# Optimization experiments

Measured on AMD Instinct MI355X. Metric: run time of the kernel, lower is better.

The kernel has to match this reference:

```python
import jax, jax.numpy as jnp
import numpy as np
import math

B, S, D, H = 1, 4096, 1024, 16
HD = D // H  # head_dim = 64


def setup_inputs() -> dict:
    key = jax.random.key(0)
    ks = jax.random.split(key, 6)
    x = jax.random.normal(ks[0], (B, S, D), dtype=jnp.float32)
    # Llama-style rotary frequencies: theta = 10000^{-2i/head_dim}
    inv_freq = 1.0 / (10000.0 ** (jnp.arange(0, HD, 2, dtype=jnp.float32) / HD))  # (HD/2,)
    t = jnp.arange(S, dtype=jnp.float32)
    freqs = jnp.outer(t, inv_freq)  # (S, HD/2)
    cos = jnp.cos(freqs)
    sin = jnp.sin(freqs)
    # additive causal mask (S, S): 0 on/below diagonal, -inf above
    mask = jnp.where(jnp.tril(jnp.ones((S, S), dtype=bool)), 0.0, -jnp.inf).astype(jnp.float32)
    scale = 1.0 / math.sqrt(D)
    wq = jax.random.normal(ks[1], (D, D), dtype=jnp.float32) * scale
    wk = jax.random.normal(ks[2], (D, D), dtype=jnp.float32) * scale
    wv = jax.random.normal(ks[3], (D, D), dtype=jnp.float32) * scale
    wo = jax.random.normal(ks[4], (D, D), dtype=jnp.float32) * scale
    return {"x": x, "cos": cos, "sin": sin, "mask": mask,
            "wq": wq, "wk": wk, "wv": wv, "wo": wo, "start_pos": 0}


def _rope(t, cos, sin):
    # t: (b, s, h, hd); cos/sin: (s, hd/2). Interleaved-pair complex rotation.
    b, s, h, hd = t.shape
    tr = t.reshape(b, s, h, hd // 2, 2)
    te, to = tr[..., 0], tr[..., 1]
    c = cos[None, :, None, :]
    sn = sin[None, :, None, :]
    oe = te * c - to * sn
    oo = te * sn + to * c
    return jnp.stack([oe, oo], axis=-1).reshape(b, s, h, hd)


def reference(x, cos, sin, mask, wq, wk, wv, wo, start_pos):
    b, s, d = x.shape
    h, hd = H, HD
    # Linear layers: y = x @ W.T (torch nn.Linear convention, W is (out,in))
    xq = (x @ wq.T).reshape(b, s, h, hd)
    xk = (x @ wk.T).reshape(b, s, h, hd)
    xv = (x @ wv.T).reshape(b, s, h, hd)
    xq = _rope(xq, cos, sin)
    xk = _rope(xk, cos, sin)
    # (b, h, s, hd)
    xq = xq.transpose(0, 2, 1, 3)
    xk = xk.transpose(0, 2, 1, 3)
    xv = xv.transpose(0, 2, 1, 3)
    scores = jnp.einsum('bhqd,bhkd->bhqk', xq, xk) / math.sqrt(hd)
    scores = scores + mask[None, None, :, :]
    attn = jax.nn.softmax(scores.astype(jnp.float32), axis=-1).astype(xq.dtype)
    out = jnp.einsum('bhqk,bhkd->bhqd', attn, xv)
    out = out.transpose(0, 2, 1, 3).reshape(b, s, d)
    return out @ wo.T
```

## Files before the change

kernel.cpp:

```cpp
#include <hip/hip_runtime.h>
#include <hip/hip_bf16.h>
#include <math.h>

typedef __bf16 bf16;
typedef __bf16 bf16x4 __attribute__((ext_vector_type(4)));
typedef __bf16 bf16x8 __attribute__((ext_vector_type(8)));
typedef float floatx4 __attribute__((ext_vector_type(4)));
typedef short short4v __attribute__((ext_vector_type(4)));

#define S_LEN 4096
#define DM 1024
#define NH 16
#define HD 64

#define GM 4096
#define GN 1024
#define GK 1024
#define FST 68

#define GLDS16(gp, lp) __builtin_amdgcn_global_load_lds( \
    (const __attribute__((address_space(1))) void*)(gp), \
    (__attribute__((address_space(3))) void*)(lp), 16, 0, 0)

__global__ void cvt_bf16(const float* __restrict__ x,  const float* __restrict__ wq,
                         const float* __restrict__ wk, const float* __restrict__ wv,
                         const float* __restrict__ wo, bf16* __restrict__ dst)
{
    size_t i4 = ((size_t)blockIdx.x * 256 + threadIdx.x) * 4;
    const float* src; size_t off;
    const size_t M1 = (size_t)1 << 20;
    if      (i4 < 4 * M1) { src = x;  off = i4;          }
    else if (i4 < 5 * M1) { src = wq; off = i4 - 4 * M1; }
    else if (i4 < 6 * M1) { src = wk; off = i4 - 5 * M1; }
    else if (i4 < 7 * M1) { src = wv; off = i4 - 6 * M1; }
    else                  { src = wo; off = i4 - 7 * M1; }
    float4 v = *(const float4*)(src + off);
    bf16x4 o = { (bf16)v.x, (bf16)v.y, (bf16)v.z, (bf16)v.w };
    *(bf16x4*)(&dst[i4]) = o;
}

template <typename CT>
__launch_bounds__(256)
__global__ void gemm_bt3(const bf16* __restrict__ A,
                         const bf16* __restrict__ B0, const bf16* __restrict__ B1,
                         const bf16* __restrict__ B2,
                         CT* __restrict__ C0, CT* __restrict__ C1, CT* __restrict__ C2)
{
    const int bz = blockIdx.z;
    const bf16* __restrict__ B = (bz == 0) ? B0 : (bz == 1 ? B1 : B2);
    CT* __restrict__ C         = (bz == 0) ? C0 : (bz == 1 ? C1 : C2);

    const int tid  = threadIdx.x;
    const int wave = tid >> 6;
    const int lane = tid & 63;
    const int wm   = (wave >> 1) * 64;
    const int wn   = (wave & 1) * 64;
    const int lrow = lane >> 4;
    const int lcol = lane & 15;

    const int m0 = blockIdx.y * 128;
    const int n0 = blockIdx.x * 128;

    __shared__ __align__(16) bf16 As[128 * 64];
    __shared__ __align__(16) bf16 Bs[128 * 64];

    floatx4 acc[4][4];
    #pragma unroll
    for (int i = 0; i < 4; i++)
        #pragma unroll
        for (int j = 0; j < 4; j++) acc[i][j] = (floatx4){0.f, 0.f, 0.f, 0.f};

    const bf16* ga0 = A + (size_t)(m0 + wave * 32 + (lane >> 3)) * GK + (lane & 7) * 8;
    const bf16* gb0 = B + (size_t)(n0 + wave * 32 + (lane >> 3)) * GK + (lane & 7) * 8;
    bf16* la = &As[(wave * 32) * 64];
    bf16* lb = &Bs[(wave * 32) * 64];

    for (int kt = 0; kt < GK; kt += 64) {
        #pragma unroll
        for (int i = 0; i < 4; i++) {
            GLDS16(ga0 + kt + (size_t)i * 8 * GK, la + i * 8 * 64);
            GLDS16(gb0 + kt + (size_t)i * 8 * GK, lb + i * 8 * 64);
        }
        __syncthreads();
        #pragma unroll
        for (int ks = 0; ks < 2; ks++) {
            bf16x8 af[4], bfr[4];
            #pragma unroll
            for (int t = 0; t < 4; t++) {
                af[t]  = *(const bf16x8*)(&As[(wm + t * 16 + lcol) * 64 + ks * 32 + lrow * 8]);
                bfr[t] = *(const bf16x8*)(&Bs[(wn + t * 16 + lcol) * 64 + ks * 32 + lrow * 8]);
            }
            #pragma unroll
            for (int mt = 0; mt < 4; mt++)
                #pragma unroll
                for (int nt = 0; nt < 4; nt++)
                    acc[mt][nt] = __builtin_amdgcn_mfma_f32_16x16x32_bf16(af[mt], bfr[nt], acc[mt][nt], 0, 0, 0);
        }
        __syncthreads();
    }

    #pragma unroll
    for (int mt = 0; mt < 4; mt++)
        #pragma unroll
        for (int nt = 0; nt < 4; nt++)
            #pragma unroll
            for (int r = 0; r < 4; r++) {
                int row = m0 + wm + mt * 16 + lrow * 4 + r;
                int col = n0 + wn + nt * 16 + lcol;
                C[(size_t)row * GN + col] = (CT)(acc[mt][nt][r]);
            }
}

__global__ void rope_kernel(bf16* __restrict__ Q, bf16* __restrict__ Kp,
                            const float* __restrict__ cosp, const float* __restrict__ sinp)
{
    int idx = blockIdx.x * 256 + threadIdx.x;
    int s = idx >> 9;
    int r = idx & 511;
    int h = r >> 5;
    int i = r & 31;
    float c  = cosp[s * 32 + i];
    float sn = sinp[s * 32 + i];
    int base = s * DM + h * 64 + 2 * i;
    float qe = (float)Q[base], qo = (float)Q[base + 1];
    Q[base]      = (bf16)(qe * c - qo * sn);
    Q[base + 1]  = (bf16)(qe * sn + qo * c);
    float ke = (float)Kp[base], ko = (float)Kp[base + 1];
    Kp[base]     = (bf16)(ke * c - ko * sn);
    Kp[base + 1] = (bf16)(ke * sn + ko * c);
}

__global__ void vtrans_kernel(const bf16* __restrict__ V, bf16* __restrict__ VT)
{
    __shared__ bf16 T[64 * 70];
    const int tid = threadIdx.x;
    const int s0  = blockIdx.x * 64;
    const int h   = blockIdx.y;
    #pragma unroll
    for (int i = 0; i < 2; i++) {
        int idx = i * 256 + tid;
        int r   = idx >> 3;
        int c   = (idx & 7) * 8;
        *(uint4*)(&T[r * 70 + c]) = *(const uint4*)(&V[(size_t)(s0 + r) * DM + h * 64 + c]);
    }
    __syncthreads();
    #pragma unroll
    for (int i = 0; i < 2; i++) {
        int idx = i * 256 + tid;
        int d   = idx >> 3;
        int c0  = (idx & 7) * 8;
        bf16x8 o;
        #pragma unroll
        for (int j = 0; j < 8; j++) o[j] = T[(c0 + j) * 70 + d];
        *(bf16x8*)(&VT[(size_t)(h * 64 + d) * S_LEN + s0 + c0]) = o;
    }
}

__launch_bounds__(256)
__global__ void flash_attn(const bf16* __restrict__ Q, const bf16* __restrict__ K,
                           const bf16* __restrict__ VT, bf16* __restrict__ O)
{
    const int bx   = blockIdx.x;
    const int h    = blockIdx.y;
    const int tid  = threadIdx.x;
    const int wave = tid >> 6;
    const int lane = tid & 63;
    const int lrow = lane >> 4;
    const int lcol = lane & 15;

    __shared__ __align__(16) bf16 Ks[2][64 * FST];
    __shared__ __align__(16) bf16 Vs[2][64 * FST];

    const float sc2 = 0.125f * 1.44269504088896340736f;

    const int  srow = tid >> 3;
    const int  sch  = (tid & 7) * 8;
    const bf16* kp  = K  + (size_t)srow * DM + h * HD + sch;
    const bf16* vp  = VT + (size_t)(h * HD + srow) * S_LEN + sch;
    const int  wof  = srow * FST + sch;

    for (int pass = 0; pass < 2; pass++) {
        const int qt = pass ? (63 - bx) : bx;
        const int q0 = qt * 64 + wave * 16;

        const bf16* qptr = Q + (size_t)(q0 + lcol) * DM + h * HD;
        bf16x8 qf[2];
        qf[0] = *(const bf16x8*)(qptr + 0 * 32 + lrow * 8);
        qf[1] = *(const bf16x8*)(qptr + 1 * 32 + lrow * 8);

        float l_lane = 0.f;
        floatx4 oacc[4];
        #pragma unroll
        for (int nt = 0; nt < 4; nt++) oacc[nt] = (floatx4){0.f, 0.f, 0.f, 0.f};

        uint4 kr0 = *(const uint4*)(kp);
        uint4 kr1 = *(const uint4*)(kp + (size_t)32 * DM);
        uint4 vr0 = *(const uint4*)(vp);
        uint4 vr1 = *(const uint4*)(vp + (size_t)32 * S_LEN);
        *(uint4*)(&Ks[0][wof])            = kr0;
        *(uint4*)(&Ks[0][wof + 32 * FST]) = kr1;
        *(uint4*)(&Vs[0][wof])            = vr0;
        *(uint4*)(&Vs[0][wof + 32 * FST]) = vr1;
        __syncthreads();

        const int ntiles = qt + 1;
        for (int t = 0; t < ntiles; t++) {
            const int cur = t & 1;
            const bool more = (t + 1 < ntiles);

            if (more) {
                size_t ko = (size_t)(t + 1) * 64 * DM;
                size_t vo = (size_t)(t + 1) * 64;
                kr0 = *(const uint4*)(kp + ko);
                kr1 = *(const uint4*)(kp + ko + (size_t)32 * DM);
                vr0 = *(const uint4*)(vp + vo);
                vr1 = *(const uint4*)(vp + vo + (size_t)32 * S_LEN);
            }

            floatx4 st[4];
            #pragma unroll
            for (int nt = 0; nt < 4; nt++) {
                floatx4 z = (floatx4){0.f, 0.f, 0.f, 0.f};
                #pragma unroll
                for (int ks = 0; ks < 2; ks++) {
                    bf16x8 kf = *(const bf16x8*)(&Ks[cur][(nt * 16 + lcol) * FST + ks * 32 + lrow * 8]);
                    z = __builtin_amdgcn_mfma_f32_16x16x32_bf16(kf, qf[ks], z, 0, 0, 0);
                }
                st[nt] = z;
            }

            if (t == qt) {
                #pragma unroll
                for (int nt = 0; nt < 4; nt++)
                    #pragma unroll
                    for (int r = 0; r < 4; r++) {
                        int kg = t * 64 + nt * 16 + lrow * 4 + r;
                        int qg = q0 + lcol;
                        float p = exp2f(st[nt][r] * sc2);
                        if (kg > qg) p = 0.f;
                        st[nt][r] = p;
                        l_lane += p;
                    }
            } else {
                #pragma unroll
                for (int nt = 0; nt < 4; nt++)
                    #pragma unroll
                    for (int r = 0; r < 4; r++) {
                        float p = exp2f(st[nt][r] * sc2);
                        st[nt][r] = p;
                        l_lane += p;
                    }
            }

            short4v pb[4];
            #pragma unroll
            for (int kt = 0; kt < 4; kt++) {
                bf16x4 pv = { (bf16)st[kt][0], (bf16)st[kt][1],
                              (bf16)st[kt][2], (bf16)st[kt][3] };
                pb[kt] = __builtin_bit_cast(short4v, pv);
            }

            #pragma unroll
            for (int nt = 0; nt < 4; nt++)
                #pragma unroll
                for (int kt = 0; kt < 4; kt++) {
                    bf16x4 va = *(const bf16x4*)(&Vs[cur][(nt * 16 + lcol) * FST + kt * 16 + lrow * 4]);
                    oacc[nt] = __builtin_amdgcn_mfma_f32_16x16x16bf16_1k(
                        __builtin_bit_cast(short4v, va), pb[kt], oacc[nt], 0, 0, 0);
                }

            if (more) {
                int nxt = cur ^ 1;
                *(uint4*)(&Ks[nxt][wof])            = kr0;
                *(uint4*)(&Ks[nxt][wof + 32 * FST]) = kr1;
                *(uint4*)(&Vs[nxt][wof])            = vr0;
                *(uint4*)(&Vs[nxt][wof + 32 * FST]) = vr1;
            }
            __syncthreads();
        }

        float l = l_lane + __shfl_xor(l_lane, 16, 64);
        l += __shfl_xor(l, 32, 64);
        float rl = 1.f / l;

        #pragma unroll
        for (int nt = 0; nt < 4; nt++) {
            bf16x4 ov = { (bf16)(oacc[nt][0] * rl), (bf16)(oacc[nt][1] * rl),
                          (bf16)(oacc[nt][2] * rl), (bf16)(oacc[nt][3] * rl) };
            *(bf16x4*)(&O[(size_t)(q0 + lcol) * DM + h * HD + nt * 16 + lrow * 4]) = ov;
        }
    }
}

extern "C" void kernel_launch(void* const* d_in, const int* in_sizes, int n_in,
                              void* d_out, int out_size, void* d_ws, size_t ws_size,
                              hipStream_t stream) {
    const float* x    = (const float*)d_in[0];
    const float* cosp = (const float*)d_in[1];
    const float* sinp = (const float*)d_in[2];
    const float* wq   = (const float*)d_in[4];
    const float* wk   = (const float*)d_in[5];
    const float* wv   = (const float*)d_in[6];
    const float* wo   = (const float*)d_in[7];
    float* out = (float*)d_out;

    const size_t SD = (size_t)S_LEN * DM;
    const size_t DD = (size_t)DM * DM;
    bf16* xb  = (bf16*)d_ws;
    bf16* wqb = xb + SD;
    bf16* wkb = wqb + DD;
    bf16* wvb = wkb + DD;
    bf16* wob = wvb + DD;
    bf16* Qw  = wob + DD;
    bf16* Kw  = Qw + SD;
    bf16* Vw  = Kw + SD;
    bf16* Aw  = Vw + SD;
    bf16* VTw = Aw + SD;

    cvt_bf16<<<8192, 256, 0, stream>>>(x, wq, wk, wv, wo, xb);
    gemm_bt3<bf16><<<dim3(GN / 128, GM / 128, 3), 256, 0, stream>>>(
        xb, wqb, wkb, wvb, Qw, Kw, Vw);
    rope_kernel<<<(S_LEN * NH * 32) / 256, 256, 0, stream>>>(Qw, Kw, cosp, sinp);
    vtrans_kernel<<<dim3(S_LEN / 64, NH), 256, 0, stream>>>(Vw, VTw);
    flash_attn<<<dim3(S_LEN / 128, NH), 256, 0, stream>>>(Qw, Kw, VTw, Aw);
    gemm_bt3<float><<<dim3(GN / 128, GM / 128, 1), 256, 0, stream>>>(
        Aw, wob, wob, wob, out, out, out);
}
```

Measured before the change: 308.7 us.

## Split attention KV range across block pairs sharing K/V tiles, combine partials

Flash attention now gives each block a pair of query tiles (qt and 63-qt) handled together, so every K/V tile loaded to shared memory serves both tiles. The KV range is split into even and odd tiles across two blocks, which doubles the grid, and each block writes unnormalized fp32 partial outputs and row sums. A new combine kernel adds the two partials, normalizes and converts to bf16. This targets low occupancy and K/V reload cost, at the price of extra fp32 workspace traffic, one more launch and higher register pressure under launch_bounds(256,4).

```diff
diff --git a/kernel.cpp b/kernel.cpp
--- a/kernel.cpp
+++ b/kernel.cpp
@@ -156,11 +156,14 @@
     }
 }
 
-__launch_bounds__(256)
+__launch_bounds__(256, 4)
 __global__ void flash_attn(const bf16* __restrict__ Q, const bf16* __restrict__ K,
-                           const bf16* __restrict__ VT, bf16* __restrict__ O)
-{
-    const int bx   = blockIdx.x;
+                           const bf16* __restrict__ VT,
+                           float* __restrict__ O0, float* __restrict__ O1,
+                           float* __restrict__ L0, float* __restrict__ L1)
+{
+    const int pi   = blockIdx.x >> 1;
+    const int p    = blockIdx.x & 1;
     const int h    = blockIdx.y;
     const int tid  = threadIdx.x;
     const int wave = tid >> 6;
@@ -168,10 +171,35 @@
     const int lrow = lane >> 4;
     const int lcol = lane & 15;
 
+    const int qtA = pi;
+    const int qtB = 63 - pi;
+
+    float* __restrict__ Op = p ? O1 : O0;
+    float* __restrict__ Lp = p ? L1 : L0;
+
     __shared__ __align__(16) bf16 Ks[2][64 * FST];
     __shared__ __align__(16) bf16 Vs[2][64 * FST];
 
     const float sc2 = 0.125f * 1.44269504088896340736f;
+
+    const int q0A = qtA * 64 + wave * 16;
+    const int q0B = qtB * 64 + wave * 16;
+
+    const bf16* qpA = Q + (size_t)(q0A + lcol) * DM + h * HD;
+    const bf16* qpB = Q + (size_t)(q0B + lcol) * DM + h * HD;
+    bf16x8 qfA[2], qfB[2];
+    qfA[0] = *(const bf16x8*)(qpA + 0 + lrow * 8);
+    qfA[1] = *(const bf16x8*)(qpA + 32 + lrow * 8);
+    qfB[0] = *(const bf16x8*)(qpB + 0 + lrow * 8);
+    qfB[1] = *(const bf16x8*)(qpB + 32 + lrow * 8);
+
+    float lA = 0.f, lB = 0.f;
+    floatx4 oaccA[4], oaccB[4];
+    #pragma unroll
+    for (int nt = 0; nt < 4; nt++) {
+        oaccA[nt] = (floatx4){0.f, 0.f, 0.f, 0.f};
+        oaccB[nt] = (floatx4){0.f, 0.f, 0.f, 0.f};
+    }
 
     const int  srow = tid >> 3;
     const int  sch  = (tid & 7) * 8;
@@ -179,117 +207,137 @@
     const bf16* vp  = VT + (size_t)(h * HD + srow) * S_LEN + sch;
     const int  wof  = srow * FST + sch;
 
-    for (int pass = 0; pass < 2; pass++) {
-        const int qt = pass ? (63 - bx) : bx;
-        const int q0 = qt * 64 + wave * 16;
-
-        const bf16* qptr = Q + (size_t)(q0 + lcol) * DM + h * HD;
-        bf16x8 qf[2];
-        qf[0] = *(const bf16x8*)(qptr + 0 * 32 + lrow * 8);
-        qf[1] = *(const bf16x8*)(qptr + 1 * 32 + lrow * 8);
-
-        float l_lane = 0.f;
-        floatx4 oacc[4];
-        #pragma unroll
-        for (int nt = 0; nt < 4; nt++) oacc[nt] = (floatx4){0.f, 0.f, 0.f, 0.f};
-
-        uint4 kr0 = *(const uint4*)(kp);
-        uint4 kr1 = *(const uint4*)(kp + (size_t)32 * DM);
-        uint4 vr0 = *(const uint4*)(vp);
-        uint4 vr1 = *(const uint4*)(vp + (size_t)32 * S_LEN);
-        *(uint4*)(&Ks[0][wof])            = kr0;
-        *(uint4*)(&Ks[0][wof + 32 * FST]) = kr1;
-        *(uint4*)(&Vs[0][wof])            = vr0;
-        *(uint4*)(&Vs[0][wof + 32 * FST]) = vr1;
-        __syncthreads();
-
-        const int ntiles = qt + 1;
-        for (int t = 0; t < ntiles; t++) {
-            const int cur = t & 1;
-            const bool more = (t + 1 < ntiles);
-
-            if (more) {
-                size_t ko = (size_t)(t + 1) * 64 * DM;
-                size_t vo = (size_t)(t + 1) * 64;
-                kr0 = *(const uint4*)(kp + ko);
-                kr1 = *(const uint4*)(kp + ko + (size_t)32 * DM);
-                vr0 = *(const uint4*)(vp + vo);
-                vr1 = *(const uint4*)(vp + vo + (size_t)32 * S_LEN);
-            }
-
-            floatx4 st[4];
-            #pragma unroll
-            for (int nt = 0; nt < 4; nt++) {
-                floatx4 z = (floatx4){0.f, 0.f, 0.f, 0.f};
+    {
+        size_t ko = (size_t)p * 64 * DM;
+        size_t vo = (size_t)p * 64;
+        uint4 a = *(const uint4*)(kp + ko);
+        uint4 b = *(const uint4*)(kp + ko + (size_t)32 * DM);
+        uint4 c = *(const uint4*)(vp + vo);
+        uint4 d = *(const uint4*)(vp + vo + (size_t)32 * S_LEN);
+        *(uint4*)(&Ks[0][wof])            = a;
+        *(uint4*)(&Ks[0][wof + 32 * FST]) = b;
+        *(uint4*)(&Vs[0][wof])            = c;
+        *(uint4*)(&Vs[0][wof + 32 * FST]) = d;
+    }
+    __syncthreads();
+
+    uint4 kr0, kr1, vr0, vr1;
+    for (int t = p; t <= qtB; t += 2) {
+        const int  cur  = ((t - p) >> 1) & 1;
+        const bool more = (t + 2 <= qtB);
+        const bool actA = (t <= qtA);
+
+        if (more) {
+            size_t ko = (size_t)(t + 2) * 64 * DM;
+            size_t vo = (size_t)(t + 2) * 64;
+            kr0 = *(const uint4*)(kp + ko);
+            kr1 = *(const uint4*)(kp + ko + (size_t)32 * DM);
+            vr0 = *(const uint4*)(vp + vo);
+            vr1 = *(const uint4*)(vp + vo + (size_t)32 * S_LEN);
+        }
+
+        short4v pbA[4], pbB[4];
+        const bool diagA = (t == qtA);
+        const bool diagB = (t == qtB);
+        #pragma unroll
+        for (int nt = 0; nt < 4; nt++) {
+            floatx4 zB = (floatx4){0.f, 0.f, 0.f, 0.f};
+            floatx4 zA = (floatx4){0.f, 0.f, 0.f, 0.f};
+            #pragma unroll
+            for (int ks = 0; ks < 2; ks++) {
+                bf16x8 kf = *(const bf16x8*)(&Ks[cur][(nt * 16 + lcol) * FST + ks * 32 + lrow * 8]);
+                zB = __builtin_amdgcn_mfma_f32_16x16x32_bf16(kf, qfB[ks], zB, 0, 0, 0);
+                if (actA)
+                    zA = __builtin_amdgcn_mfma_f32_16x16x32_bf16(kf, qfA[ks], zA, 0, 0, 0);
+            }
+            if (diagB) {
                 #pragma unroll
-                for (int ks = 0; ks < 2; ks++) {
-                    bf16x8 kf = *(const bf16x8*)(&Ks[cur][(nt * 16 + lcol) * FST + ks * 32 + lrow * 8]);
-                    z = __builtin_amdgcn_mfma_f32_16x16x32_bf16(kf, qf[ks], z, 0, 0, 0);
+                for (int r = 0; r < 4; r++) {
+                    int kg = t * 64 + nt * 16 + lrow * 4 + r;
+                    float pr = exp2f(zB[r] * sc2);
+                    if (kg > q0B + lcol) pr = 0.f;
+                    zB[r] = pr; lB += pr;
                 }
-                st[nt] = z;
-            }
-
-            if (t == qt) {
+            } else {
                 #pragma unroll
-                for (int nt = 0; nt < 4; nt++)
+                for (int r = 0; r < 4; r++) {
+                    float pr = exp2f(zB[r] * sc2);
+                    zB[r] = pr; lB += pr;
+                }
+            }
+            bf16x4 pvB = { (bf16)zB[0], (bf16)zB[1], (bf16)zB[2], (bf16)zB[3] };
+            pbB[nt] = __builtin_bit_cast(short4v, pvB);
+            if (actA) {
+                if (diagA) {
                     #pragma unroll
                     for (int r = 0; r < 4; r++) {
                         int kg = t * 64 + nt * 16 + lrow * 4 + r;
-                        int qg = q0 + lcol;
-                        float p = exp2f(st[nt][r] * sc2);
-                        if (kg > qg) p = 0.f;
-                        st[nt][r] = p;
-                        l_lane += p;
+                        float pr = exp2f(zA[r] * sc2);
+                        if (kg > q0A + lcol) pr = 0.f;
+                        zA[r] = pr; lA += pr;
                     }
-            } else {
-                #pragma unroll
-                for (int nt = 0; nt < 4; nt++)
+                } else {
                     #pragma unroll
                     for (int r = 0; r < 4; r++) {
-                        float p = exp2f(st[nt][r] * sc2);
-                        st[nt][r] = p;
-                        l_lane += p;
+                        float pr = exp2f(zA[r] * sc2);
+                        zA[r] = pr; lA += pr;
                     }
-            }
-
-            short4v pb[4];
+                }
+                bf16x4 pvA = { (bf16)zA[0], (bf16)zA[1], (bf16)zA[2], (bf16)zA[3] };
+                pbA[nt] = __builtin_bit_cast(short4v, pvA);
+            }
+        }
+
+        #pragma unroll
+        for (int nt = 0; nt < 4; nt++)
             #pragma unroll
             for (int kt = 0; kt < 4; kt++) {
-                bf16x4 pv = { (bf16)st[kt][0], (bf16)st[kt][1],
-                              (bf16)st[kt][2], (bf16)st[kt][3] };
-                pb[kt] = __builtin_bit_cast(short4v, pv);
-            }
-
-            #pragma unroll
-            for (int nt = 0; nt < 4; nt++)
-                #pragma unroll
-                for (int kt = 0; kt < 4; kt++) {
-                    bf16x4 va = *(const bf16x4*)(&Vs[cur][(nt * 16 + lcol) * FST + kt * 16 + lrow * 4]);
-                    oacc[nt] = __builtin_amdgcn_mfma_f32_16x16x16bf16_1k(
-                        __builtin_bit_cast(short4v, va), pb[kt], oacc[nt], 0, 0, 0);
-                }
-
-            if (more) {
-                int nxt = cur ^ 1;
-                *(uint4*)(&Ks[nxt][wof])            = kr0;
-                *(uint4*)(&Ks[nxt][wof + 32 * FST]) = kr1;
-                *(uint4*)(&Vs[nxt][wof])            = vr0;
-                *(uint4*)(&Vs[nxt][wof + 32 * FST]) = vr1;
-            }
-            __syncthreads();
-        }
-
-        float l = l_lane + __shfl_xor(l_lane, 16, 64);
-        l += __shfl_xor(l, 32, 64);
-        float rl = 1.f / l;
-
-        #pragma unroll
-        for (int nt = 0; nt < 4; nt++) {
-            bf16x4 ov = { (bf16)(oacc[nt][0] * rl), (bf16)(oacc[nt][1] * rl),
-                          (bf16)(oacc[nt][2] * rl), (bf16)(oacc[nt][3] * rl) };
-            *(bf16x4*)(&O[(size_t)(q0 + lcol) * DM + h * HD + nt * 16 + lrow * 4]) = ov;
-        }
-    }
+                bf16x4 va = *(const bf16x4*)(&Vs[cur][(nt * 16 + lcol) * FST + kt * 16 + lrow * 4]);
+                short4v vas = __builtin_bit_cast(short4v, va);
+                oaccB[nt] = __builtin_amdgcn_mfma_f32_16x16x16bf16_1k(vas, pbB[kt], oaccB[nt], 0, 0, 0);
+                if (actA)
+                    oaccA[nt] = __builtin_amdgcn_mfma_f32_16x16x16bf16_1k(vas, pbA[kt], oaccA[nt], 0, 0, 0);
+            }
+
+        if (more) {
+            int nxt = cur ^ 1;
+            *(uint4*)(&Ks[nxt][wof])            = kr0;
+            *(uint4*)(&Ks[nxt][wof + 32 * FST]) = kr1;
+            *(uint4*)(&Vs[nxt][wof])            = vr0;
+            *(uint4*)(&Vs[nxt][wof + 32 * FST]) = vr1;
+        }
+        __syncthreads();
+    }
+
+    lA += __shfl_xor(lA, 16, 64);
+    lA += __shfl_xor(lA, 32, 64);
+    lB += __shfl_xor(lB, 16, 64);
+    lB += __shfl_xor(lB, 32, 64);
+    if (lrow == 0) {
+        Lp[h * S_LEN + q0A + lcol] = lA;
+        Lp[h * S_LEN + q0B + lcol] = lB;
+    }
+    #pragma unroll
+    for (int nt = 0; nt < 4; nt++) {
+        *(floatx4*)(&Op[(size_t)(q0A + lcol) * DM + h * HD + nt * 16 + lrow * 4]) = oaccA[nt];
+        *(floatx4*)(&Op[(size_t)(q0B + lcol) * DM + h * HD + nt * 16 + lrow * 4]) = oaccB[nt];
+    }
+}
+
+__global__ void combine_kernel(const float* __restrict__ O0, const float* __restrict__ O1,
+                               const float* __restrict__ L0, const float* __restrict__ L1,
+                               bf16* __restrict__ Aw)
+{
+    int i4 = (blockIdx.x * 256 + threadIdx.x) * 4;
+    int q = i4 >> 10;
+    int c = i4 & 1023;
+    int h = c >> 6;
+    float rl = 1.f / (L0[h * S_LEN + q] + L1[h * S_LEN + q]);
+    float4 a = *(const float4*)(O0 + i4);
+    float4 b = *(const float4*)(O1 + i4);
+    bf16x4 o = { (bf16)((a.x + b.x) * rl), (bf16)((a.y + b.y) * rl),
+                 (bf16)((a.z + b.z) * rl), (bf16)((a.w + b.w) * rl) };
+    *(bf16x4*)(&Aw[i4]) = o;
 }
 
 extern "C" void kernel_launch(void* const* d_in, const int* in_sizes, int n_in,
@@ -316,13 +364,18 @@
     bf16* Vw  = Kw + SD;
     bf16* Aw  = Vw + SD;
     bf16* VTw = Aw + SD;
+    float* O0f = (float*)(VTw + SD);
+    float* O1f = O0f + SD;
+    float* L0f = O1f + SD;
+    float* L1f = L0f + (size_t)S_LEN * NH;
 
     cvt_bf16<<<8192, 256, 0, stream>>>(x, wq, wk, wv, wo, xb);
     gemm_bt3<bf16><<<dim3(GN / 128, GM / 128, 3), 256, 0, stream>>>(
         xb, wqb, wkb, wvb, Qw, Kw, Vw);
     rope_kernel<<<(S_LEN * NH * 32) / 256, 256, 0, stream>>>(Qw, Kw, cosp, sinp);
     vtrans_kernel<<<dim3(S_LEN / 64, NH), 256, 0, stream>>>(Vw, VTw);
-    flash_attn<<<dim3(S_LEN / 128, NH), 256, 0, stream>>>(Qw, Kw, VTw, Aw);
+    flash_attn<<<dim3(64, NH), 256, 0, stream>>>(Qw, Kw, VTw, O0f, O1f, L0f, L1f);
+    combine_kernel<<<S_LEN * DM / 1024, 256, 0, stream>>>(O0f, O1f, L0f, L1f, Aw);
     gemm_bt3<float><<<dim3(GN / 128, GM / 128, 1), 256, 0, stream>>>(
         Aw, wob, wob, wob, out, out, out);
 }
```

Measured after the change: 306.9 us. No clear change (-0.6%).
